# Optimization experiments

Hardware: AMD Instinct MI355X
Metric: run time of the kernel (lower is better)

The kernel has to match this reference:

```python
import jax, jax.numpy as jnp
import numpy as np

N, F_IN, H1, H2, HEADS, E = 8192, 512, 128, 64, 3, 262144
NEG_SLOPE = 0.2  # PyG GATConv default negative_slope


def _add_self_loops(src, dst, n):
    loop = jnp.arange(n, dtype=src.dtype)
    return jnp.concatenate([src, loop]), jnp.concatenate([dst, loop])


def _gcn_conv(x, src, dst, W, b, n):
    # PyG GCNConv: h = x @ W, add self-loops, symmetric D^-1/2 A D^-1/2 aggregation, + bias
    h = x @ W
    s, d = _add_self_loops(src, dst, n)
    deg = jax.ops.segment_sum(jnp.ones(s.shape, h.dtype), d, num_segments=n)
    dinv = jnp.where(deg > 0, jax.lax.rsqrt(deg), 0.0)
    norm = dinv[s] * dinv[d]  # [E']
    return jax.ops.segment_sum(h[s] * norm[:, None], d, num_segments=n) + b


def _gat_conv(x, src, dst, W, a_src, a_dst, b, n, heads, concat):
    # PyG GATConv: per-head linear, LeakyReLU attention logits, segment softmax over
    # incoming edges per destination node, weighted scatter-aggregate.
    out_dim = W.shape[1] // heads
    h = (x @ W).reshape(n, heads, out_dim)  # [N, H, D]
    s, d = _add_self_loops(src, dst, n)
    a_s = jnp.einsum('nhd,hd->nh', h, a_src)
    a_d = jnp.einsum('nhd,hd->nh', h, a_dst)
    e = jax.nn.leaky_relu(a_s[s] + a_d[d], NEG_SLOPE)  # [E', H]
    m = jax.ops.segment_max(e, d, num_segments=n)      # stable softmax per dst segment
    ex = jnp.exp(e - m[d])
    den = jax.ops.segment_sum(ex, d, num_segments=n)
    msg = h[s] * (ex / den[d])[..., None]              # [E', H, D]
    out = jax.ops.segment_sum(msg, d, num_segments=n)  # [N, H, D]
    if concat:
        return out.reshape(n, heads * out_dim) + b
    return out.mean(axis=1) + b


def _forward(x, edge_index, gcn_W1, gcn_b1, gcn_Wmu, gcn_bmu, gcn_Wlv, gcn_blv,
             gat_W1, gat_as1, gat_ad1, gat_b1,
             gat_Wmu, gat_asmu, gat_admu, gat_bmu,
             gat_Wlv, gat_aslv, gat_adlv, gat_blv,
             eps_gcn, eps_gat):
    src, dst = edge_index[0], edge_index[1]
    n = x.shape[0]
    mu_g = lv_g = z_g = None
    for i in range(gcn_W1.shape[0]):  # gcn branches
        h = jax.nn.relu(_gcn_conv(x, src, dst, gcn_W1[i], gcn_b1[i], n))
        mu = _gcn_conv(h, src, dst, gcn_Wmu[i], gcn_bmu[i], n)
        lv = _gcn_conv(h, src, dst, gcn_Wlv[i], gcn_blv[i], n)
        z = mu + eps_gcn[i] * jnp.exp(lv)  # faithful: logvar passed as logstd
        mu_g = mu if mu_g is None else jnp.maximum(mu_g, mu)
        lv_g = lv if lv_g is None else jnp.maximum(lv_g, lv)
        z_g = z if z_g is None else jnp.maximum(z_g, z)
    mu_a = lv_a = z_a = None
    for i in range(gat_W1.shape[0]):  # gat branches
        h = jax.nn.relu(_gat_conv(x, src, dst, gat_W1[i], gat_as1[i], gat_ad1[i], gat_b1[i], n, HEADS, True))
        mu = _gat_conv(h, src, dst, gat_Wmu[i], gat_asmu[i], gat_admu[i], gat_bmu[i], n, HEADS, False)
        lv = _gat_conv(h, src, dst, gat_Wlv[i], gat_aslv[i], gat_adlv[i], gat_blv[i], n, HEADS, False)
        z = mu + eps_gat[i] * jnp.exp(lv)
        mu_a = mu if mu_a is None else jnp.maximum(mu_a, mu)
        lv_a = lv if lv_a is None else jnp.maximum(lv_a, lv)
        z_a = z if z_a is None else jnp.maximum(z_a, z)
    mu_max = jnp.maximum(mu_g, mu_a)
    lv_max = jnp.maximum(lv_g, lv_a)
    z_max = jnp.maximum(z_g, z_a)
    adj = jax.nn.sigmoid(z_max @ z_max.T)  # InnerProductDecoder.forward_all(sigmoid=True)
    return adj, mu_max, lv_max


def setup_inputs():
    key = jax.random.key(0)
    ki = iter(jax.random.split(key, 32))
    p = lambda shape: jax.random.normal(next(ki), shape, dtype=jnp.float32) * 0.05
    x = jax.random.normal(next(ki), (N, F_IN), dtype=jnp.float32)
    edge_index = jax.random.randint(next(ki), (2, E), 0, N)
    return dict(
        x=x, edge_index=edge_index,
        gcn_W1=p((2, F_IN, H1)), gcn_b1=p((2, H1)),
        gcn_Wmu=p((2, H1, H2)), gcn_bmu=p((2, H2)),
        gcn_Wlv=p((2, H1, H2)), gcn_blv=p((2, H2)),
        gat_W1=p((2, F_IN, HEADS * H1)), gat_as1=p((2, HEADS, H1)),
        gat_ad1=p((2, HEADS, H1)), gat_b1=p((2, HEADS * H1)),
        gat_Wmu=p((2, HEADS * H1, HEADS * H2)), gat_asmu=p((2, HEADS, H2)),
        gat_admu=p((2, HEADS, H2)), gat_bmu=p((2, H2)),
        gat_Wlv=p((2, HEADS * H1, HEADS * H2)), gat_aslv=p((2, HEADS, H2)),
        gat_adlv=p((2, HEADS, H2)), gat_blv=p((2, H2)),
        eps_gcn=jax.random.normal(next(ki), (2, N, H2), dtype=jnp.float32),
        eps_gat=jax.random.normal(next(ki), (2, N, H2), dtype=jnp.float32),
    )


def reference(x, edge_index, gcn_W1, gcn_b1, gcn_Wmu, gcn_bmu, gcn_Wlv, gcn_blv,
              gat_W1, gat_as1, gat_ad1, gat_b1,
              gat_Wmu, gat_asmu, gat_admu, gat_bmu,
              gat_Wlv, gat_aslv, gat_adlv, gat_blv,
              eps_gcn, eps_gat):
    return _forward(x, edge_index, gcn_W1, gcn_b1, gcn_Wmu, gcn_bmu, gcn_Wlv, gcn_blv,
                    gat_W1, gat_as1, gat_ad1, gat_b1,
                    gat_Wmu, gat_asmu, gat_admu, gat_bmu,
                    gat_Wlv, gat_aslv, gat_adlv, gat_blv,
                    eps_gcn, eps_gat)
```

## Files before the change

### kernel.cpp

```cpp
#include <hip/hip_runtime.h>
#include <hip/hip_bf16.h>
#include <math.h>
#include <stddef.h>

#define NN 8192
#define NHEAD 3
#define NEG_SLOPE 0.2f

typedef __attribute__((ext_vector_type(8))) short short8;
typedef __attribute__((ext_vector_type(4))) float f32x4;

__device__ __forceinline__ float lrelu(float x) { return x > 0.f ? x : NEG_SLOPE * x; }
__device__ __forceinline__ float sigf(float x) { return 1.f / (1.f + __expf(-x)); }

__device__ __forceinline__ void splitbf(float x, unsigned short& hu, unsigned short& lu) {
    __hip_bfloat16 h = __float2bfloat16(x);
    float hf = __bfloat162float(h);
    __hip_bfloat16 l = __float2bfloat16(x - hf);
    hu = *reinterpret_cast<unsigned short*>(&h);
    lu = *reinterpret_cast<unsigned short*>(&l);
}
__device__ __forceinline__ unsigned short bfr(float x) {
    __hip_bfloat16 h = __float2bfloat16(x);
    return *reinterpret_cast<unsigned short*>(&h);
}
__device__ __forceinline__ unsigned int pack2(float a, float b) {
    return (unsigned int)bfr(a) | ((unsigned int)bfr(b) << 16);
}
__device__ __forceinline__ float2 unpk(unsigned int v) {
    unsigned int lo = v << 16;
    unsigned int hi = v & 0xffff0000u;
    float2 r;
    r.x = *reinterpret_cast<float*>(&lo);
    r.y = *reinterpret_cast<float*>(&hi);
    return r;
}
__device__ __forceinline__ float bf2f(unsigned short u) {
    unsigned int b = (unsigned int)u << 16;
    return *reinterpret_cast<float*>(&b);
}

__device__ __forceinline__ void gll16(const unsigned short* g, unsigned short* l) {
    __builtin_amdgcn_global_load_lds(
        (const __attribute__((address_space(1))) unsigned int*)g,
        (__attribute__((address_space(3))) unsigned int*)l, 16, 0, 0);
}

__global__ void k_zero(int* __restrict__ p, int n) {
    int i = blockIdx.x * blockDim.x + threadIdx.x;
    if (i < n) p[i] = 0;
}
__global__ void k_count(const int* __restrict__ dst, int* __restrict__ cnt, int E) {
    int i = blockIdx.x * blockDim.x + threadIdx.x;
    if (i < E) atomicAdd(&cnt[dst[i]], 1);
}
__global__ void k_dinv(const int* __restrict__ cnt, float* __restrict__ dinv) {
    int i = blockIdx.x * blockDim.x + threadIdx.x;
    if (i < NN) dinv[i] = rsqrtf((float)(cnt[i] + 1));
}
__global__ void k_scan(const int* __restrict__ cnt, int* __restrict__ row_ptr) {
    __shared__ int part[1024];
    int t = threadIdx.x;
    int base = t * 8;
    int loc[8];
    int s = 0;
    #pragma unroll
    for (int j = 0; j < 8; ++j) { loc[j] = s; s += cnt[base + j]; }
    part[t] = s;
    __syncthreads();
    for (int off = 1; off < 1024; off <<= 1) {
        int v = (t >= off) ? part[t - off] : 0;
        __syncthreads();
        part[t] += v;
        __syncthreads();
    }
    int pre = (t == 0) ? 0 : part[t - 1];
    #pragma unroll
    for (int j = 0; j < 8; ++j) row_ptr[base + j] = pre + loc[j];
    if (t == 1023) row_ptr[NN] = part[1023];
}
__global__ void k_fill(const int* __restrict__ src, const int* __restrict__ dst,
                       const int* __restrict__ row_ptr, int* __restrict__ cursor,
                       int* __restrict__ csr_src, int E) {
    int i = blockIdx.x * blockDim.x + threadIdx.x;
    if (i < E) {
        int d = dst[i];
        csr_src[row_ptr[d] + atomicAdd(&cursor[d], 1)] = src[i];
    }
}

__global__ void k_split_x(const float* __restrict__ x, unsigned short* __restrict__ x2) {
    int i = blockIdx.x * 256 + threadIdx.x;
    int m = i >> 7, k4 = (i & 127) * 4;
    float4 v = *(const float4*)(x + (size_t)m * 512 + k4);
    unsigned short h[4], l[4];
    splitbf(v.x, h[0], l[0]); splitbf(v.y, h[1], l[1]);
    splitbf(v.z, h[2], l[2]); splitbf(v.w, h[3], l[3]);
    ushort4 hv; hv.x = h[0]; hv.y = h[1]; hv.z = h[2]; hv.w = h[3];
    ushort4 lv; lv.x = l[0]; lv.y = l[1]; lv.z = l[2]; lv.w = l[3];
    *(ushort4*)&x2[(size_t)m * 1024 + k4] = hv;
    *(ushort4*)&x2[(size_t)m * 1024 + 512 + k4] = lv;
}

__global__ void k_wsplitT(const float* __restrict__ W, unsigned short* __restrict__ Wt,
                          int K, int N, size_t wt_z_stride, int noff, int noff_z) {
    int b = blockIdx.z;
    W += (size_t)b * K * N;
    Wt += (size_t)b * wt_z_stride;
    int rowbase = noff + b * noff_z;
    int k0 = blockIdx.x * 32, n0 = blockIdx.y * 32;
    __shared__ float tl[32][33];
    int tid = threadIdx.x;
    int r = tid >> 5, cc = tid & 31;
    #pragma unroll
    for (int c = 0; c < 4; ++c)
        tl[r + c * 8][cc] = W[(size_t)(k0 + r + c * 8) * N + n0 + cc];
    __syncthreads();
    #pragma unroll
    for (int c = 0; c < 4; ++c) {
        int n = r + c * 8, k = cc;
        float xv = tl[k][n];
        unsigned short h, l;
        splitbf(xv, h, l);
        size_t ro = (size_t)(rowbase + n0 + n) * 2 * K;
        Wt[ro + k0 + k] = h;
        Wt[ro + K + k0 + k] = l;
    }
}

template <int ROWS>
__device__ __forceinline__ void stage(const unsigned short* __restrict__ gbase, int lda,
                                      unsigned short* lds, int wid, int lane) {
    #pragma unroll
    for (int c = 0; c < ROWS / 32; ++c) {
        int chunk = c * 4 + wid;
        int row = chunk * 8 + (lane >> 3);
        int g = (lane & 7) ^ (row & 7);
        gll16(gbase + (size_t)row * lda + g * 8, lds + chunk * 512);
    }
}
__device__ __forceinline__ short8 fragr(const unsigned short* lds, int row, int kg) {
    return *(const short8*)(lds + row * 64 + ((kg ^ (row & 7)) * 8));
}

template <int EPI>
__global__ __launch_bounds__(256) void k_gemm2(
    const unsigned short* __restrict__ A2, size_t azs, int lda,
    const unsigned short* __restrict__ B2, size_t bzs, int ldb,
    void* __restrict__ Cv, size_t czs, int ldc, int K) {
    __shared__ __align__(16) unsigned short sAh[128 * 64];
    __shared__ __align__(16) unsigned short sAl[128 * 64];
    __shared__ __align__(16) unsigned short sBh[64 * 64];
    __shared__ __align__(16) unsigned short sBl[64 * 64];
    const int tid = threadIdx.x;
    const int wid = tid >> 6, lane = tid & 63;
    const int wr = wid >> 1, wc = wid & 1;
    const int lr = lane & 15, lg = lane >> 4;
    const int m0 = blockIdx.x * 128, n0 = blockIdx.y * 64;
    const int z = blockIdx.z;
    A2 += (size_t)z * azs;
    B2 += (size_t)z * bzs;

    const f32x4 zero4 = {0.f, 0.f, 0.f, 0.f};
    f32x4 acc[4][2];
    #pragma unroll
    for (int m = 0; m < 4; ++m)
        #pragma unroll
        for (int n = 0; n < 2; ++n) acc[m][n] = zero4;

    for (int k0 = 0; k0 < K; k0 += 64) {
        stage<128>(A2 + (size_t)m0 * lda + k0,     lda, sAh, wid, lane);
        stage<128>(A2 + (size_t)m0 * lda + K + k0, lda, sAl, wid, lane);
        stage<64> (B2 + (size_t)n0 * ldb + k0,     ldb, sBh, wid, lane);
        stage<64> (B2 + (size_t)n0 * ldb + K + k0, ldb, sBl, wid, lane);
        __syncthreads();
        #pragma unroll
        for (int ks = 0; ks < 2; ++ks) {
            const int kg = ks * 4 + lg;
            short8 ah[4], al[4], bh[2], bl[2];
            #pragma unroll
            for (int m = 0; m < 4; ++m) {
                int row = wr * 64 + m * 16 + lr;
                ah[m] = fragr(sAh, row, kg);
                al[m] = fragr(sAl, row, kg);
            }
            #pragma unroll
            for (int n = 0; n < 2; ++n) {
                int row = wc * 32 + n * 16 + lr;
                bh[n] = fragr(sBh, row, kg);
                bl[n] = fragr(sBl, row, kg);
            }
            #pragma unroll
            for (int m = 0; m < 4; ++m)
                #pragma unroll
                for (int n = 0; n < 2; ++n) {
                    acc[m][n] = __builtin_amdgcn_mfma_f32_16x16x32_bf16(ah[m], bh[n], acc[m][n], 0, 0, 0);
                    acc[m][n] = __builtin_amdgcn_mfma_f32_16x16x32_bf16(al[m], bh[n], acc[m][n], 0, 0, 0);
                    acc[m][n] = __builtin_amdgcn_mfma_f32_16x16x32_bf16(ah[m], bl[n], acc[m][n], 0, 0, 0);
                }
        }
        __syncthreads();
    }
    #pragma unroll
    for (int m = 0; m < 4; ++m)
        #pragma unroll
        for (int n = 0; n < 2; ++n)
            #pragma unroll
            for (int j = 0; j < 4; ++j) {
                int row = m0 + wr * 64 + m * 16 + lg * 4 + j;
                int col = n0 + wc * 32 + n * 16 + lr;
                float o = acc[m][n][j];
                if (EPI == 1) {
                    ((float*)Cv + (size_t)z * czs)[(size_t)row * ldc + col] = sigf(o);
                } else if (EPI == 2) {
                    ((unsigned short*)Cv + (size_t)z * czs)[(size_t)row * ldc + col] = bfr(o);
                } else {
                    ((float*)Cv + (size_t)z * czs)[(size_t)row * ldc + col] = o;
                }
            }
}

__global__ void k_gcn_a1(const unsigned int* __restrict__ xwb, const float* __restrict__ dinv,
                         const int* __restrict__ rp, const int* __restrict__ cs,
                         const float* __restrict__ b1, unsigned int* __restrict__ hb) {
    int d = blockIdx.x;
    int t = threadIdx.x;
    float dd = dinv[d];
    float2 sv = unpk(xwb[(size_t)d * 128 + t]);
    float a0 = dd * sv.x, a1 = dd * sv.y;
    int e0 = rp[d], e1 = rp[d + 1];
    int j = e0;
    for (; j + 4 <= e1; j += 4) {
        int s0 = cs[j], s1 = cs[j + 1], s2 = cs[j + 2], s3 = cs[j + 3];
        float w0 = dinv[s0], w1 = dinv[s1], w2 = dinv[s2], w3 = dinv[s3];
        float2 v0 = unpk(xwb[(size_t)s0 * 128 + t]);
        float2 v1 = unpk(xwb[(size_t)s1 * 128 + t]);
        float2 v2 = unpk(xwb[(size_t)s2 * 128 + t]);
        float2 v3 = unpk(xwb[(size_t)s3 * 128 + t]);
        a0 += w0 * v0.x + w1 * v1.x + w2 * v2.x + w3 * v3.x;
        a1 += w0 * v0.y + w1 * v1.y + w2 * v2.y + w3 * v3.y;
    }
    for (; j < e1; ++j) {
        int s = cs[j];
        float w = dinv[s];
        float2 v = unpk(xwb[(size_t)s * 128 + t]);
        a0 += w * v.x;
        a1 += w * v.y;
    }
    float o0 = fmaxf(dd * a0 + b1[2 * t], 0.f);
    float o1 = fmaxf(dd * a1 + b1[2 * t + 1], 0.f);
    hb[(size_t)d * 128 + t] = pack2(o0, o1);
}

__global__ void k_gcn_a2(const unsigned int* __restrict__ hb, const float* __restrict__ dinv,
                         const int* __restrict__ rp, const int* __restrict__ cs,
                         unsigned int* __restrict__ hA2u) {
    int d = blockIdx.x;
    int t = threadIdx.x;
    float dd = dinv[d];
    float2 sv = unpk(hb[(size_t)d * 128 + t]);
    float a0 = dd * sv.x, a1 = dd * sv.y;
    int e0 = rp[d], e1 = rp[d + 1];
    int j = e0;
    for (; j + 4 <= e1; j += 4) {
        int s0 = cs[j], s1 = cs[j + 1], s2 = cs[j + 2], s3 = cs[j + 3];
        float w0 = dinv[s0], w1 = dinv[s1], w2 = dinv[s2], w3 = dinv[s3];
        float2 v0 = unpk(hb[(size_t)s0 * 128 + t]);
        float2 v1 = unpk(hb[(size_t)s1 * 128 + t]);
        float2 v2 = unpk(hb[(size_t)s2 * 128 + t]);
        float2 v3 = unpk(hb[(size_t)s3 * 128 + t]);
        a0 += w0 * v0.x + w1 * v1.x + w2 * v2.x + w3 * v3.x;
        a1 += w0 * v0.y + w1 * v1.y + w2 * v2.y + w3 * v3.y;
    }
    for (; j < e1; ++j) {
        int s = cs[j];
        float w = dinv[s];
        float2 v = unpk(hb[(size_t)s * 128 + t]);
        a0 += w * v.x;
        a1 += w * v.y;
    }
    float o0 = dd * a0, o1 = dd * a1;
    int br = t >> 6, cu = t & 63;
    unsigned short h0, l0, h1, l1;
    splitbf(o0, h0, l0);
    splitbf(o1, h1, l1);
    hA2u[(size_t)d * 256 + br * 128 + cu] = (unsigned int)h0 | ((unsigned int)h1 << 16);
    hA2u[(size_t)d * 256 + br * 128 + 64 + cu] = (unsigned int)l0 | ((unsigned int)l1 << 16);
}

__global__ void k_gat_log1(const unsigned int* __restrict__ xwb, const float* __restrict__ a_s,
                           const float* __restrict__ a_d, float* __restrict__ as_n,
                           float* __restrict__ ad_n) {
    int br = blockIdx.z;
    int n = blockIdx.x;
    int hd = threadIdx.x >> 6, lane = threadIdx.x & 63;
    const unsigned int* hp = xwb + (size_t)n * 384 + br * 192 + hd * 64;
    const float* av = a_s + br * 384 + hd * 128;
    const float* dv = a_d + br * 384 + hd * 128;
    float2 f = unpk(hp[lane]);
    float ss = f.x * av[2 * lane] + f.y * av[2 * lane + 1];
    float sd = f.x * dv[2 * lane] + f.y * dv[2 * lane + 1];
    #pragma unroll
    for (int off = 32; off; off >>= 1) {
        ss += __shfl_down(ss, off);
        sd += __shfl_down(sd, off);
    }
    if (lane == 0) {
        as_n[(size_t)br * NN * 3 + n * 3 + hd] = ss;
        ad_n[(size_t)br * NN * 3 + n * 3 + hd] = sd;
    }
}

__global__ void k_gat_log2(const unsigned short* __restrict__ h2gb, const float* __restrict__ asmu,
                           const float* __restrict__ aslv, const float* __restrict__ admu,
                           const float* __restrict__ adlv, float* __restrict__ as_n,
                           float* __restrict__ ad_n) {
    int zz = blockIdx.z;
    int br = zz >> 1, mt = zz & 1;
    int n = blockIdx.x;
    int hd = threadIdx.x >> 6, lane = threadIdx.x & 63;
    const unsigned short* hp = h2gb + (size_t)br * NN * 384 + (size_t)n * 384 + mt * 192 + hd * 64;
    const float* av = (mt ? aslv : asmu) + br * 192 + hd * 64;
    const float* dv = (mt ? adlv : admu) + br * 192 + hd * 64;
    float hv = bf2f(hp[lane]);
    float ss = hv * av[lane];
    float sd = hv * dv[lane];
    #pragma unroll
    for (int off = 32; off; off >>= 1) {
        ss += __shfl_down(ss, off);
        sd += __shfl_down(sd, off);
    }
    if (lane == 0) {
        as_n[(size_t)zz * NN * 3 + n * 3 + hd] = ss;
        ad_n[(size_t)zz * NN * 3 + n * 3 + hd] = sd;
    }
}

__global__ void k_gat_attn(const float* __restrict__ as_n, const float* __restrict__ ad_n,
                           const int* __restrict__ rp, const int* __restrict__ cs,
                           float* __restrict__ w_csr, float* __restrict__ w_self, int E3) {
    int zz = blockIdx.z;
    as_n += (size_t)zz * NN * 3;
    ad_n += (size_t)zz * NN * 3;
    w_csr += (size_t)zz * E3;
    w_self += (size_t)zz * NN * 3;
    int d = blockIdx.x;
    int hd = threadIdx.x >> 6, lane = threadIdx.x & 63;
    int e0 = rp[d], e1 = rp[d + 1];
    float add = ad_n[d * 3 + hd];
    float eself = lrelu(as_n[d * 3 + hd] + add);
    float mx = eself;
    for (int j = e0 + lane; j < e1; j += 64) {
        float e = lrelu(as_n[cs[j] * 3 + hd] + add);
        w_csr[(size_t)j * 3 + hd] = e;
        mx = fmaxf(mx, e);
    }
    #pragma unroll
    for (int off = 32; off; off >>= 1) mx = fmaxf(mx, __shfl_xor(mx, off));
    float sm = (lane == 0) ? __expf(eself - mx) : 0.f;
    for (int j = e0 + lane; j < e1; j += 64)
        sm += __expf(w_csr[(size_t)j * 3 + hd] - mx);
    #pragma unroll
    for (int off = 32; off; off >>= 1) sm += __shfl_xor(sm, off);
    float inv = 1.f / sm;
    if (lane == 0) w_self[d * 3 + hd] = __expf(eself - mx) * inv;
    for (int j = e0 + lane; j < e1; j += 64)
        w_csr[(size_t)j * 3 + hd] = __expf(w_csr[(size_t)j * 3 + hd] - mx) * inv;
}

__global__ void k_gat_agg1(const unsigned int* __restrict__ xwb, const float* __restrict__ w_csr,
                           const float* __restrict__ w_self, const int* __restrict__ rp,
                           const int* __restrict__ cs, const float* __restrict__ b1,
                           unsigned int* __restrict__ h1su, int E3) {
    int d = blockIdx.x;
    int t = threadIdx.x;
    int br = t >= 192 ? 1 : 0;
    int cu = t - br * 192;
    int hd = cu >> 6;
    const float* wc = w_csr + (size_t)br * E3;
    float ws = w_self[(size_t)br * NN * 3 + d * 3 + hd];
    float2 sv = unpk(xwb[(size_t)d * 384 + t]);
    float a0 = ws * sv.x, a1 = ws * sv.y;
    int e0 = rp[d], e1 = rp[d + 1];
    int j = e0;
    for (; j + 4 <= e1; j += 4) {
        int s0 = cs[j], s1 = cs[j + 1], s2 = cs[j + 2], s3 = cs[j + 3];
        float w0 = wc[(size_t)(j + 0) * 3 + hd];
        float w1 = wc[(size_t)(j + 1) * 3 + hd];
        float w2 = wc[(size_t)(j + 2) * 3 + hd];
        float w3 = wc[(size_t)(j + 3) * 3 + hd];
        float2 v0 = unpk(xwb[(size_t)s0 * 384 + t]);
        float2 v1 = unpk(xwb[(size_t)s1 * 384 + t]);
        float2 v2 = unpk(xwb[(size_t)s2 * 384 + t]);
        float2 v3 = unpk(xwb[(size_t)s3 * 384 + t]);
        a0 += w0 * v0.x + w1 * v1.x + w2 * v2.x + w3 * v3.x;
        a1 += w0 * v0.y + w1 * v1.y + w2 * v2.y + w3 * v3.y;
    }
    for (; j < e1; ++j) {
        int s = cs[j];
        float w = wc[(size_t)j * 3 + hd];
        float2 v = unpk(xwb[(size_t)s * 384 + t]);
        a0 += w * v.x;
        a1 += w * v.y;
    }
    float o0 = fmaxf(a0 + b1[br * 384 + 2 * cu], 0.f);
    float o1 = fmaxf(a1 + b1[br * 384 + 2 * cu + 1], 0.f);
    unsigned short h0, l0, h1, l1;
    splitbf(o0, h0, l0);
    splitbf(o1, h1, l1);
    h1su[(size_t)d * 768 + br * 384 + cu] = (unsigned int)h0 | ((unsigned int)h1 << 16);
    h1su[(size_t)d * 768 + br * 384 + 192 + cu] = (unsigned int)l0 | ((unsigned int)l1 << 16);
}

__global__ void k_gat_agg2(const unsigned int* __restrict__ h2gu, const float* __restrict__ w_csr,
                           const float* __restrict__ w_self, const int* __restrict__ rp,
                           const int* __restrict__ cs, const float* __restrict__ bmu,
                           const float* __restrict__ blv, float* __restrict__ mt_gat, int E3) {
    int br = blockIdx.z;
    int d = blockIdx.x;
    int t = threadIdx.x;
    int mt = t >= 96 ? 1 : 0;
    int cu = t - mt * 96;
    int hd = cu >> 5;
    const unsigned int* hp = h2gu + (size_t)br * NN * 192;
    const float* wc = w_csr + (size_t)(br * 2 + mt) * E3;
    float ws = w_self[(size_t)(br * 2 + mt) * NN * 3 + d * 3 + hd];
    float2 sv = unpk(hp[(size_t)d * 192 + t]);
    float a0 = ws * sv.x, a1 = ws * sv.y;
    int e0 = rp[d], e1 = rp[d + 1];
    int j = e0;
    for (; j + 4 <= e1; j += 4) {
        int s0 = cs[j], s1 = cs[j + 1], s2 = cs[j + 2], s3 = cs[j + 3];
        float w0 = wc[(size_t)(j + 0) * 3 + hd];
        float w1 = wc[(size_t)(j + 1) * 3 + hd];
        float w2 = wc[(size_t)(j + 2) * 3 + hd];
        float w3 = wc[(size_t)(j + 3) * 3 + hd];
        float2 v0 = unpk(hp[(size_t)s0 * 192 + t]);
        float2 v1 = unpk(hp[(size_t)s1 * 192 + t]);
        float2 v2 = unpk(hp[(size_t)s2 * 192 + t]);
        float2 v3 = unpk(hp[(size_t)s3 * 192 + t]);
        a0 += w0 * v0.x + w1 * v1.x + w2 * v2.x + w3 * v3.x;
        a1 += w0 * v0.y + w1 * v1.y + w2 * v2.y + w3 * v3.y;
    }
    for (; j < e1; ++j) {
        int s = cs[j];
        float w = wc[(size_t)j * 3 + hd];
        float2 v = unpk(hp[(size_t)s * 192 + t]);
        a0 += w * v.x;
        a1 += w * v.y;
    }
    __shared__ float red[384];
    red[2 * t] = a0;
    red[2 * t + 1] = a1;
    __syncthreads();
    if (t < 128) {
        int mt2 = t >> 6, dd = t & 63;
        float tot = red[mt2 * 192 + dd] + red[mt2 * 192 + 64 + dd] + red[mt2 * 192 + 128 + dd];
        const float* bias = mt2 ? blv : bmu;
        float o = tot * (1.f / 3.f) + bias[br * 64 + dd];
        mt_gat[((size_t)(br * 2 + mt2) * NN + d) * 64 + dd] = o;
    }
}

__global__ void k_finalize(const float* __restrict__ muv_gcn, const float* __restrict__ gcn_bmu,
                           const float* __restrict__ gcn_blv, const float* __restrict__ mt_gat,
                           const float* __restrict__ eps_gcn, const float* __restrict__ eps_gat,
                           float* __restrict__ mu_o, float* __restrict__ lv_o,
                           unsigned short* __restrict__ z2) {
    int i = blockIdx.x * 256 + threadIdx.x;
    int d = i >> 6, c = i & 63;
    const size_t NN64 = (size_t)NN * 64;
    float mu, lv, zm;
    {
        float m = muv_gcn[(size_t)d * 128 + c] + gcn_bmu[c];
        float l = muv_gcn[(size_t)d * 128 + 64 + c] + gcn_blv[c];
        float z = m + eps_gcn[i] * __expf(l);
        mu = m; lv = l; zm = z;
    }
    {
        float m = muv_gcn[NN64 * 2 + (size_t)d * 128 + c] + gcn_bmu[64 + c];
        float l = muv_gcn[NN64 * 2 + (size_t)d * 128 + 64 + c] + gcn_blv[64 + c];
        float z = m + eps_gcn[NN64 + i] * __expf(l);
        mu = fmaxf(mu, m); lv = fmaxf(lv, l); zm = fmaxf(zm, z);
    }
    #pragma unroll
    for (int br = 0; br < 2; ++br) {
        float m = mt_gat[(size_t)(br * 2 + 0) * NN64 + i];
        float l = mt_gat[(size_t)(br * 2 + 1) * NN64 + i];
        float z = m + eps_gat[(size_t)br * NN64 + i] * __expf(l);
        mu = fmaxf(mu, m); lv = fmaxf(lv, l); zm = fmaxf(zm, z);
    }
    mu_o[i] = mu;
    lv_o[i] = lv;
    unsigned short hh, ll;
    splitbf(zm, hh, ll);
    z2[(size_t)d * 128 + c] = hh;
    z2[(size_t)d * 128 + 64 + c] = ll;
}

extern "C" void kernel_launch(void* const* d_in, const int* in_sizes, int n_in,
                              void* d_out, int out_size, void* d_ws, size_t ws_size,
                              hipStream_t stream) {
    const float* x  = (const float*)d_in[0];
    const int*   ei = (const int*)d_in[1];
    const int E = in_sizes[1] / 2;
    const int E3 = E * 3;
    const int* src = ei;
    const int* dst = ei + E;

    const float* gcn_W1  = (const float*)d_in[2];
    const float* gcn_b1  = (const float*)d_in[3];
    const float* gcn_Wmu = (const float*)d_in[4];
    const float* gcn_bmu = (const float*)d_in[5];
    const float* gcn_Wlv = (const float*)d_in[6];
    const float* gcn_blv = (const float*)d_in[7];
    const float* gat_W1  = (const float*)d_in[8];
    const float* gat_as1 = (const float*)d_in[9];
    const float* gat_ad1 = (const float*)d_in[10];
    const float* gat_b1  = (const float*)d_in[11];
    const float* gat_Wmu = (const float*)d_in[12];
    const float* gat_asmu= (const float*)d_in[13];
    const float* gat_admu= (const float*)d_in[14];
    const float* gat_bmu = (const float*)d_in[15];
    const float* gat_Wlv = (const float*)d_in[16];
    const float* gat_aslv= (const float*)d_in[17];
    const float* gat_adlv= (const float*)d_in[18];
    const float* gat_blv = (const float*)d_in[19];
    const float* eps_gcn = (const float*)d_in[20];
    const float* eps_gat = (const float*)d_in[21];

    char* p = (char*)d_ws;
    auto alloc = [&](size_t bytes) {
        void* r = (void*)p;
        p += (bytes + 255) & ~(size_t)255;
        return r;
    };
    int*   cnt     = (int*)alloc((size_t)NN * 4);
    int*   cursor  = (int*)alloc((size_t)NN * 4);
    int*   row_ptr = (int*)alloc((size_t)(NN + 1) * 4);
    int*   csr_src = (int*)alloc((size_t)E * 4);
    float* dinv    = (float*)alloc((size_t)NN * 4);
    float* as_n1   = (float*)alloc((size_t)2 * NN * 3 * 4);
    float* ad_n1   = (float*)alloc((size_t)2 * NN * 3 * 4);
    float* wself1  = (float*)alloc((size_t)2 * NN * 3 * 4);
    float* wcsr1   = (float*)alloc((size_t)2 * E3 * 4);
    float* as_n2   = (float*)alloc((size_t)4 * NN * 3 * 4);
    float* ad_n2   = (float*)alloc((size_t)4 * NN * 3 * 4);
    float* wself2  = (float*)alloc((size_t)4 * NN * 3 * 4);
    float* wcsr2   = (float*)alloc((size_t)4 * E3 * 4);
    unsigned short* x2       = (unsigned short*)alloc((size_t)NN * 1024 * 2);
    unsigned short* wt_gcn1  = (unsigned short*)alloc((size_t)256 * 1024 * 2);
    unsigned short* wt_gcnmuv= (unsigned short*)alloc((size_t)2 * 128 * 256 * 2);
    unsigned short* wt_gat1  = (unsigned short*)alloc((size_t)768 * 1024 * 2);
    unsigned short* wt_gatmuv= (unsigned short*)alloc((size_t)2 * 384 * 768 * 2);
    unsigned int* xwb  = (unsigned int*)alloc((size_t)NN * 384 * 4);
    unsigned int* hb   = (unsigned int*)alloc((size_t)NN * 128 * 4);
    unsigned int* hA2u = (unsigned int*)alloc((size_t)NN * 256 * 4);
    float* muv_gcn = (float*)alloc((size_t)2 * NN * 128 * 4);
    unsigned int* h1su = (unsigned int*)alloc((size_t)NN * 768 * 4);
    unsigned short* h2gb = (unsigned short*)alloc((size_t)2 * NN * 384 * 2);
    float* mt_gat  = (float*)alloc((size_t)4 * NN * 64 * 4);
    unsigned short* z2 = (unsigned short*)alloc((size_t)NN * 128 * 2);

    float* adj  = (float*)d_out;
    float* mu_o = adj + (size_t)NN * NN;
    float* lv_o = mu_o + (size_t)NN * 64;

    k_zero<<<(2 * NN + 255) / 256, 256, 0, stream>>>(cnt, 2 * NN);
    k_count<<<(E + 255) / 256, 256, 0, stream>>>(dst, cnt, E);
    k_dinv<<<(NN + 255) / 256, 256, 0, stream>>>(cnt, dinv);
    k_scan<<<1, 1024, 0, stream>>>(cnt, row_ptr);
    k_fill<<<(E + 255) / 256, 256, 0, stream>>>(src, dst, row_ptr, cursor, csr_src, E);

    k_split_x<<<NN * 512 / 4 / 256, 256, 0, stream>>>(x, x2);
    k_wsplitT<<<dim3(16, 4, 2), 256, 0, stream>>>(gcn_W1, wt_gcn1, 512, 128, 0, 0, 128);
    k_wsplitT<<<dim3(4, 2, 2), 256, 0, stream>>>(gcn_Wmu, wt_gcnmuv, 128, 64,
                                                 (size_t)128 * 256, 0, 0);
    k_wsplitT<<<dim3(4, 2, 2), 256, 0, stream>>>(gcn_Wlv, wt_gcnmuv, 128, 64,
                                                 (size_t)128 * 256, 64, 0);
    k_wsplitT<<<dim3(16, 12, 2), 256, 0, stream>>>(gat_W1, wt_gat1, 512, 384, 0, 0, 384);
    k_wsplitT<<<dim3(12, 6, 2), 256, 0, stream>>>(gat_Wmu, wt_gatmuv, 384, 192,
                                                  (size_t)384 * 768, 0, 0);
    k_wsplitT<<<dim3(12, 6, 2), 256, 0, stream>>>(gat_Wlv, wt_gatmuv, 384, 192,
                                                  (size_t)384 * 768, 192, 0);

    k_gemm2<2><<<dim3(64, 4, 1), 256, 0, stream>>>(x2, 0, 1024, wt_gcn1, 0, 1024,
                                                   xwb, 0, 256, 512);
    k_gcn_a1<<<NN, 128, 0, stream>>>(xwb, dinv, row_ptr, csr_src, gcn_b1, hb);
    k_gcn_a2<<<NN, 128, 0, stream>>>(hb, dinv, row_ptr, csr_src, hA2u);
    k_gemm2<0><<<dim3(64, 2, 2), 256, 0, stream>>>((const unsigned short*)hA2u, 256, 512,
                                                   wt_gcnmuv, (size_t)128 * 256, 256,
                                                   muv_gcn, (size_t)NN * 128, 128, 128);

    k_gemm2<2><<<dim3(64, 12, 1), 256, 0, stream>>>(x2, 0, 1024, wt_gat1, 0, 1024,
                                                    xwb, 0, 768, 512);
    k_gat_log1<<<dim3(NN, 1, 2), 192, 0, stream>>>(xwb, gat_as1, gat_ad1, as_n1, ad_n1);
    k_gat_attn<<<dim3(NN, 1, 2), 192, 0, stream>>>(as_n1, ad_n1, row_ptr, csr_src,
                                                   wcsr1, wself1, E3);
    k_gat_agg1<<<NN, 384, 0, stream>>>(xwb, wcsr1, wself1, row_ptr, csr_src, gat_b1,
                                       h1su, E3);
    k_gemm2<2><<<dim3(64, 6, 2), 256, 0, stream>>>((const unsigned short*)h1su, 768, 1536,
                                                   wt_gatmuv, (size_t)384 * 768, 768,
                                                   h2gb, (size_t)NN * 384, 384, 384);
    k_gat_log2<<<dim3(NN, 1, 4), 192, 0, stream>>>(h2gb, gat_asmu, gat_aslv, gat_admu,
                                                   gat_adlv, as_n2, ad_n2);
    k_gat_attn<<<dim3(NN, 1, 4), 192, 0, stream>>>(as_n2, ad_n2, row_ptr, csr_src,
                                                   wcsr2, wself2, E3);
    k_gat_agg2<<<dim3(NN, 1, 2), 192, 0, stream>>>((const unsigned int*)h2gb, wcsr2, wself2,
                                                   row_ptr, csr_src, gat_bmu, gat_blv,
                                                   mt_gat, E3);

    k_finalize<<<NN * 64 / 256, 256, 0, stream>>>(muv_gcn, gcn_bmu, gcn_blv, mt_gat,
                                                  eps_gcn, eps_gat, mu_o, lv_o, z2);
    k_gemm2<1><<<dim3(64, 128, 1), 256, 0, stream>>>(z2, 0, 128, z2, 0, 128,
                                                     adj, 0, NN, 64);
}
```

Measured before the change: 390.2 us.

## Switch intermediate GEMMs from split-bf16 three-term to single fp16 MFMA

Replaces the hi/lo bf16 split (three MFMAs per tile) with a single fp16 term for the feature GEMMs, keeping three-term split only for the final z·zᵀ adjacency GEMM. This halves the staged operand traffic and removes two thirds of MFMA work in those GEMMs and halves weight/activation buffers. The aggregation kernels are rewritten to process four fp16 values per thread with uint2 loads, and gat_agg2 merges both branches into one block. Accuracy drops because of fp16 range and mantissa limits compared with the split representation.

```diff
diff --git a/kernel.cpp b/kernel.cpp
--- a/kernel.cpp
+++ b/kernel.cpp
@@ -4,40 +4,40 @@
 #include <stddef.h>
 
 #define NN 8192
-#define NHEAD 3
 #define NEG_SLOPE 0.2f
 
-typedef __attribute__((ext_vector_type(8))) short short8;
+typedef _Float16 h8 __attribute__((ext_vector_type(8)));
 typedef __attribute__((ext_vector_type(4))) float f32x4;
 
 __device__ __forceinline__ float lrelu(float x) { return x > 0.f ? x : NEG_SLOPE * x; }
 __device__ __forceinline__ float sigf(float x) { return 1.f / (1.f + __expf(-x)); }
 
-__device__ __forceinline__ void splitbf(float x, unsigned short& hu, unsigned short& lu) {
-    __hip_bfloat16 h = __float2bfloat16(x);
-    float hf = __bfloat162float(h);
-    __hip_bfloat16 l = __float2bfloat16(x - hf);
-    hu = *reinterpret_cast<unsigned short*>(&h);
-    lu = *reinterpret_cast<unsigned short*>(&l);
-}
-__device__ __forceinline__ unsigned short bfr(float x) {
-    __hip_bfloat16 h = __float2bfloat16(x);
-    return *reinterpret_cast<unsigned short*>(&h);
-}
-__device__ __forceinline__ unsigned int pack2(float a, float b) {
-    return (unsigned int)bfr(a) | ((unsigned int)bfr(b) << 16);
-}
-__device__ __forceinline__ float2 unpk(unsigned int v) {
-    unsigned int lo = v << 16;
-    unsigned int hi = v & 0xffff0000u;
+__device__ __forceinline__ unsigned short f16b(float x) {
+    _Float16 h = (_Float16)x;
+    unsigned short u;
+    __builtin_memcpy(&u, &h, 2);
+    return u;
+}
+__device__ __forceinline__ float f16f(unsigned short u) {
+    _Float16 h;
+    __builtin_memcpy(&h, &u, 2);
+    return (float)h;
+}
+__device__ __forceinline__ void splith(float x, unsigned short& hu, unsigned short& lu) {
+    _Float16 h = (_Float16)x;
+    float hf = (float)h;
+    _Float16 l = (_Float16)(x - hf);
+    __builtin_memcpy(&hu, &h, 2);
+    __builtin_memcpy(&lu, &l, 2);
+}
+__device__ __forceinline__ float2 unpkh(unsigned int v) {
     float2 r;
-    r.x = *reinterpret_cast<float*>(&lo);
-    r.y = *reinterpret_cast<float*>(&hi);
+    r.x = f16f((unsigned short)(v & 0xffffu));
+    r.y = f16f((unsigned short)(v >> 16));
     return r;
 }
-__device__ __forceinline__ float bf2f(unsigned short u) {
-    unsigned int b = (unsigned int)u << 16;
-    return *reinterpret_cast<float*>(&b);
+__device__ __forceinline__ unsigned int packh(float a, float b) {
+    return (unsigned int)f16b(a) | ((unsigned int)f16b(b) << 16);
 }
 
 __device__ __forceinline__ void gll16(const unsigned short* g, unsigned short* l) {
@@ -89,21 +89,17 @@
     }
 }
 
-__global__ void k_split_x(const float* __restrict__ x, unsigned short* __restrict__ x2) {
+__global__ void k_cvt_x(const float* __restrict__ x, unsigned short* __restrict__ xh) {
     int i = blockIdx.x * 256 + threadIdx.x;
     int m = i >> 7, k4 = (i & 127) * 4;
     float4 v = *(const float4*)(x + (size_t)m * 512 + k4);
-    unsigned short h[4], l[4];
-    splitbf(v.x, h[0], l[0]); splitbf(v.y, h[1], l[1]);
-    splitbf(v.z, h[2], l[2]); splitbf(v.w, h[3], l[3]);
-    ushort4 hv; hv.x = h[0]; hv.y = h[1]; hv.z = h[2]; hv.w = h[3];
-    ushort4 lv; lv.x = l[0]; lv.y = l[1]; lv.z = l[2]; lv.w = l[3];
-    *(ushort4*)&x2[(size_t)m * 1024 + k4] = hv;
-    *(ushort4*)&x2[(size_t)m * 1024 + 512 + k4] = lv;
-}
-
-__global__ void k_wsplitT(const float* __restrict__ W, unsigned short* __restrict__ Wt,
-                          int K, int N, size_t wt_z_stride, int noff, int noff_z) {
+    ushort4 o;
+    o.x = f16b(v.x); o.y = f16b(v.y); o.z = f16b(v.z); o.w = f16b(v.w);
+    *(ushort4*)&xh[(size_t)m * 512 + k4] = o;
+}
+
+__global__ void k_wT(const float* __restrict__ W, unsigned short* __restrict__ Wt,
+                     int K, int N, size_t wt_z_stride, int noff, int noff_z) {
     int b = blockIdx.z;
     W += (size_t)b * K * N;
     Wt += (size_t)b * wt_z_stride;
@@ -119,12 +115,7 @@
     #pragma unroll
     for (int c = 0; c < 4; ++c) {
         int n = r + c * 8, k = cc;
-        float xv = tl[k][n];
-        unsigned short h, l;
-        splitbf(xv, h, l);
-        size_t ro = (size_t)(rowbase + n0 + n) * 2 * K;
-        Wt[ro + k0 + k] = h;
-        Wt[ro + K + k0 + k] = l;
+        Wt[(size_t)(rowbase + n0 + n) * K + k0 + k] = f16b(tl[k][n]);
     }
 }
 
@@ -139,19 +130,19 @@
         gll16(gbase + (size_t)row * lda + g * 8, lds + chunk * 512);
     }
 }
-__device__ __forceinline__ short8 fragr(const unsigned short* lds, int row, int kg) {
-    return *(const short8*)(lds + row * 64 + ((kg ^ (row & 7)) * 8));
-}
-
-template <int EPI>
+__device__ __forceinline__ h8 fragrh(const unsigned short* lds, int row, int kg) {
+    return *(const h8*)(lds + row * 64 + ((kg ^ (row & 7)) * 8));
+}
+
+template <int TERMS, int EPI>
 __global__ __launch_bounds__(256) void k_gemm2(
     const unsigned short* __restrict__ A2, size_t azs, int lda,
     const unsigned short* __restrict__ B2, size_t bzs, int ldb,
     void* __restrict__ Cv, size_t czs, int ldc, int K) {
     __shared__ __align__(16) unsigned short sAh[128 * 64];
-    __shared__ __align__(16) unsigned short sAl[128 * 64];
     __shared__ __align__(16) unsigned short sBh[64 * 64];
-    __shared__ __align__(16) unsigned short sBl[64 * 64];
+    __shared__ __align__(16) unsigned short sAl[(TERMS == 3) ? 128 * 64 : 8];
+    __shared__ __align__(16) unsigned short sBl[(TERMS == 3) ? 64 * 64 : 8];
     const int tid = threadIdx.x;
     const int wid = tid >> 6, lane = tid & 63;
     const int wr = wid >> 1, wc = wid & 1;
@@ -169,34 +160,38 @@
         for (int n = 0; n < 2; ++n) acc[m][n] = zero4;
 
     for (int k0 = 0; k0 < K; k0 += 64) {
-        stage<128>(A2 + (size_t)m0 * lda + k0,     lda, sAh, wid, lane);
-        stage<128>(A2 + (size_t)m0 * lda + K + k0, lda, sAl, wid, lane);
-        stage<64> (B2 + (size_t)n0 * ldb + k0,     ldb, sBh, wid, lane);
-        stage<64> (B2 + (size_t)n0 * ldb + K + k0, ldb, sBl, wid, lane);
+        stage<128>(A2 + (size_t)m0 * lda + k0, lda, sAh, wid, lane);
+        stage<64> (B2 + (size_t)n0 * ldb + k0, ldb, sBh, wid, lane);
+        if (TERMS == 3) {
+            stage<128>(A2 + (size_t)m0 * lda + K + k0, lda, sAl, wid, lane);
+            stage<64> (B2 + (size_t)n0 * ldb + K + k0, ldb, sBl, wid, lane);
+        }
         __syncthreads();
         #pragma unroll
         for (int ks = 0; ks < 2; ++ks) {
             const int kg = ks * 4 + lg;
-            short8 ah[4], al[4], bh[2], bl[2];
+            h8 ah[4], al[4], bh[2], bl[2];
             #pragma unroll
             for (int m = 0; m < 4; ++m) {
                 int row = wr * 64 + m * 16 + lr;
-                ah[m] = fragr(sAh, row, kg);
-                al[m] = fragr(sAl, row, kg);
+                ah[m] = fragrh(sAh, row, kg);
+                if (TERMS == 3) al[m] = fragrh(sAl, row, kg);
             }
             #pragma unroll
             for (int n = 0; n < 2; ++n) {
                 int row = wc * 32 + n * 16 + lr;
-                bh[n] = fragr(sBh, row, kg);
-                bl[n] = fragr(sBl, row, kg);
+                bh[n] = fragrh(sBh, row, kg);
+                if (TERMS == 3) bl[n] = fragrh(sBl, row, kg);
             }
             #pragma unroll
             for (int m = 0; m < 4; ++m)
                 #pragma unroll
                 for (int n = 0; n < 2; ++n) {
-                    acc[m][n] = __builtin_amdgcn_mfma_f32_16x16x32_bf16(ah[m], bh[n], acc[m][n], 0, 0, 0);
-                    acc[m][n] = __builtin_amdgcn_mfma_f32_16x16x32_bf16(al[m], bh[n], acc[m][n], 0, 0, 0);
-                    acc[m][n] = __builtin_amdgcn_mfma_f32_16x16x32_bf16(ah[m], bl[n], acc[m][n], 0, 0, 0);
+                    acc[m][n] = __builtin_amdgcn_mfma_f32_16x16x32_f16(ah[m], bh[n], acc[m][n], 0, 0, 0);
+                    if (TERMS == 3) {
+                        acc[m][n] = __builtin_amdgcn_mfma_f32_16x16x32_f16(al[m], bh[n], acc[m][n], 0, 0, 0);
+                        acc[m][n] = __builtin_amdgcn_mfma_f32_16x16x32_f16(ah[m], bl[n], acc[m][n], 0, 0, 0);
+                    }
                 }
         }
         __syncthreads();
@@ -213,91 +208,112 @@
                 if (EPI == 1) {
                     ((float*)Cv + (size_t)z * czs)[(size_t)row * ldc + col] = sigf(o);
                 } else if (EPI == 2) {
-                    ((unsigned short*)Cv + (size_t)z * czs)[(size_t)row * ldc + col] = bfr(o);
+                    ((unsigned short*)Cv + (size_t)z * czs)[(size_t)row * ldc + col] = f16b(o);
                 } else {
                     ((float*)Cv + (size_t)z * czs)[(size_t)row * ldc + col] = o;
                 }
             }
 }
 
-__global__ void k_gcn_a1(const unsigned int* __restrict__ xwb, const float* __restrict__ dinv,
+__global__ void k_gcn_a1(const uint2* __restrict__ xw2, const float* __restrict__ dinv,
                          const int* __restrict__ rp, const int* __restrict__ cs,
-                         const float* __restrict__ b1, unsigned int* __restrict__ hb) {
+                         const float* __restrict__ b1, uint2* __restrict__ hb2) {
     int d = blockIdx.x;
     int t = threadIdx.x;
     float dd = dinv[d];
-    float2 sv = unpk(xwb[(size_t)d * 128 + t]);
-    float a0 = dd * sv.x, a1 = dd * sv.y;
+    uint2 sv = xw2[(size_t)d * 64 + t];
+    float2 s0 = unpkh(sv.x), s1 = unpkh(sv.y);
+    float a0 = dd * s0.x, a1 = dd * s0.y, a2 = dd * s1.x, a3 = dd * s1.y;
     int e0 = rp[d], e1 = rp[d + 1];
     int j = e0;
     for (; j + 4 <= e1; j += 4) {
-        int s0 = cs[j], s1 = cs[j + 1], s2 = cs[j + 2], s3 = cs[j + 3];
-        float w0 = dinv[s0], w1 = dinv[s1], w2 = dinv[s2], w3 = dinv[s3];
-        float2 v0 = unpk(xwb[(size_t)s0 * 128 + t]);
-        float2 v1 = unpk(xwb[(size_t)s1 * 128 + t]);
-        float2 v2 = unpk(xwb[(size_t)s2 * 128 + t]);
-        float2 v3 = unpk(xwb[(size_t)s3 * 128 + t]);
-        a0 += w0 * v0.x + w1 * v1.x + w2 * v2.x + w3 * v3.x;
-        a1 += w0 * v0.y + w1 * v1.y + w2 * v2.y + w3 * v3.y;
+        int i0 = cs[j], i1 = cs[j + 1], i2 = cs[j + 2], i3 = cs[j + 3];
+        float w0 = dinv[i0], w1 = dinv[i1], w2 = dinv[i2], w3 = dinv[i3];
+        uint2 v0 = xw2[(size_t)i0 * 64 + t];
+        uint2 v1 = xw2[(size_t)i1 * 64 + t];
+        uint2 v2 = xw2[(size_t)i2 * 64 + t];
+        uint2 v3 = xw2[(size_t)i3 * 64 + t];
+        float2 p;
+        p = unpkh(v0.x); a0 += w0 * p.x; a1 += w0 * p.y;
+        p = unpkh(v0.y); a2 += w0 * p.x; a3 += w0 * p.y;
+        p = unpkh(v1.x); a0 += w1 * p.x; a1 += w1 * p.y;
+        p = unpkh(v1.y); a2 += w1 * p.x; a3 += w1 * p.y;
+        p = unpkh(v2.x); a0 += w2 * p.x; a1 += w2 * p.y;
+        p = unpkh(v2.y); a2 += w2 * p.x; a3 += w2 * p.y;
+        p = unpkh(v3.x); a0 += w3 * p.x; a1 += w3 * p.y;
+        p = unpkh(v3.y); a2 += w3 * p.x; a3 += w3 * p.y;
     }
     for (; j < e1; ++j) {
         int s = cs[j];
         float w = dinv[s];
-        float2 v = unpk(xwb[(size_t)s * 128 + t]);
-        a0 += w * v.x;
-        a1 += w * v.y;
-    }
-    float o0 = fmaxf(dd * a0 + b1[2 * t], 0.f);
-    float o1 = fmaxf(dd * a1 + b1[2 * t + 1], 0.f);
-    hb[(size_t)d * 128 + t] = pack2(o0, o1);
-}
-
-__global__ void k_gcn_a2(const unsigned int* __restrict__ hb, const float* __restrict__ dinv,
+        uint2 v = xw2[(size_t)s * 64 + t];
+        float2 p;
+        p = unpkh(v.x); a0 += w * p.x; a1 += w * p.y;
+        p = unpkh(v.y); a2 += w * p.x; a3 += w * p.y;
+    }
+    int c = 4 * t;
+    float o0 = fmaxf(dd * a0 + b1[c], 0.f);
+    float o1 = fmaxf(dd * a1 + b1[c + 1], 0.f);
+    float o2 = fmaxf(dd * a2 + b1[c + 2], 0.f);
+    float o3 = fmaxf(dd * a3 + b1[c + 3], 0.f);
+    uint2 o;
+    o.x = packh(o0, o1);
+    o.y = packh(o2, o3);
+    hb2[(size_t)d * 64 + t] = o;
+}
+
+__global__ void k_gcn_a2(const uint2* __restrict__ hb2, const float* __restrict__ dinv,
                          const int* __restrict__ rp, const int* __restrict__ cs,
-                         unsigned int* __restrict__ hA2u) {
+                         uint2* __restrict__ hA2) {
     int d = blockIdx.x;
     int t = threadIdx.x;
     float dd = dinv[d];
-    float2 sv = unpk(hb[(size_t)d * 128 + t]);
-    float a0 = dd * sv.x, a1 = dd * sv.y;
+    uint2 sv = hb2[(size_t)d * 64 + t];
+    float2 s0 = unpkh(sv.x), s1 = unpkh(sv.y);
+    float a0 = dd * s0.x, a1 = dd * s0.y, a2 = dd * s1.x, a3 = dd * s1.y;
     int e0 = rp[d], e1 = rp[d + 1];
     int j = e0;
     for (; j + 4 <= e1; j += 4) {
-        int s0 = cs[j], s1 = cs[j + 1], s2 = cs[j + 2], s3 = cs[j + 3];
-        float w0 = dinv[s0], w1 = dinv[s1], w2 = dinv[s2], w3 = dinv[s3];
-        float2 v0 = unpk(hb[(size_t)s0 * 128 + t]);
-        float2 v1 = unpk(hb[(size_t)s1 * 128 + t]);
-        float2 v2 = unpk(hb[(size_t)s2 * 128 + t]);
-        float2 v3 = unpk(hb[(size_t)s3 * 128 + t]);
-        a0 += w0 * v0.x + w1 * v1.x + w2 * v2.x + w3 * v3.x;
-        a1 += w0 * v0.y + w1 * v1.y + w2 * v2.y + w3 * v3.y;
+        int i0 = cs[j], i1 = cs[j + 1], i2 = cs[j + 2], i3 = cs[j + 3];
+        float w0 = dinv[i0], w1 = dinv[i1], w2 = dinv[i2], w3 = dinv[i3];
+        uint2 v0 = hb2[(size_t)i0 * 64 + t];
+        uint2 v1 = hb2[(size_t)i1 * 64 + t];
+        uint2 v2 = hb2[(size_t)i2 * 64 + t];
+        uint2 v3 = hb2[(size_t)i3 * 64 + t];
+        float2 p;
+        p = unpkh(v0.x); a0 += w0 * p.x; a1 += w0 * p.y;
+        p = unpkh(v0.y); a2 += w0 * p.x; a3 += w0 * p.y;
+        p = unpkh(v1.x); a0 += w1 * p.x; a1 += w1 * p.y;
+        p = unpkh(v1.y); a2 += w1 * p.x; a3 += w1 * p.y;
+        p = unpkh(v2.x); a0 += w2 * p.x; a1 += w2 * p.y;
+        p = unpkh(v2.y); a2 += w2 * p.x; a3 += w2 * p.y;
+        p = unpkh(v3.x); a0 += w3 * p.x; a1 += w3 * p.y;
+        p = unpkh(v3.y); a2 += w3 * p.x; a3 += w3 * p.y;
     }
     for (; j < e1; ++j) {
         int s = cs[j];
         float w = dinv[s];
-        float2 v = unpk(hb[(size_t)s * 128 + t]);
-        a0 += w * v.x;
-        a1 += w * v.y;
-    }
-    float o0 = dd * a0, o1 = dd * a1;
-    int br = t >> 6, cu = t & 63;
-    unsigned short h0, l0, h1, l1;
-    splitbf(o0, h0, l0);
-    splitbf(o1, h1, l1);
-    hA2u[(size_t)d * 256 + br * 128 + cu] = (unsigned int)h0 | ((unsigned int)h1 << 16);
-    hA2u[(size_t)d * 256 + br * 128 + 64 + cu] = (unsigned int)l0 | ((unsigned int)l1 << 16);
-}
-
-__global__ void k_gat_log1(const unsigned int* __restrict__ xwb, const float* __restrict__ a_s,
+        uint2 v = hb2[(size_t)s * 64 + t];
+        float2 p;
+        p = unpkh(v.x); a0 += w * p.x; a1 += w * p.y;
+        p = unpkh(v.y); a2 += w * p.x; a3 += w * p.y;
+    }
+    uint2 o;
+    o.x = packh(dd * a0, dd * a1);
+    o.y = packh(dd * a2, dd * a3);
+    hA2[(size_t)d * 64 + t] = o;
+}
+
+__global__ void k_gat_log1(const unsigned int* __restrict__ xwu, const float* __restrict__ a_s,
                            const float* __restrict__ a_d, float* __restrict__ as_n,
                            float* __restrict__ ad_n) {
     int br = blockIdx.z;
     int n = blockIdx.x;
     int hd = threadIdx.x >> 6, lane = threadIdx.x & 63;
-    const unsigned int* hp = xwb + (size_t)n * 384 + br * 192 + hd * 64;
+    const unsigned int* hp = xwu + (size_t)n * 384 + br * 192 + hd * 64;
     const float* av = a_s + br * 384 + hd * 128;
     const float* dv = a_d + br * 384 + hd * 128;
-    float2 f = unpk(hp[lane]);
+    float2 f = unpkh(hp[lane]);
     float ss = f.x * av[2 * lane] + f.y * av[2 * lane + 1];
     float sd = f.x * dv[2 * lane] + f.y * dv[2 * lane + 1];
     #pragma unroll
@@ -322,7 +338,7 @@
     const unsigned short* hp = h2gb + (size_t)br * NN * 384 + (size_t)n * 384 + mt * 192 + hd * 64;
     const float* av = (mt ? aslv : asmu) + br * 192 + hd * 64;
     const float* dv = (mt ? adlv : admu) + br * 192 + hd * 64;
-    float hv = bf2f(hp[lane]);
+    float hv = f16f(hp[lane]);
     float ss = hv * av[lane];
     float sd = hv * dv[lane];
     #pragma unroll
@@ -368,97 +384,123 @@
         w_csr[(size_t)j * 3 + hd] = __expf(w_csr[(size_t)j * 3 + hd] - mx) * inv;
 }
 
-__global__ void k_gat_agg1(const unsigned int* __restrict__ xwb, const float* __restrict__ w_csr,
+__global__ void k_gat_agg1(const uint2* __restrict__ xw2, const float* __restrict__ w_csr,
                            const float* __restrict__ w_self, const int* __restrict__ rp,
                            const int* __restrict__ cs, const float* __restrict__ b1,
-                           unsigned int* __restrict__ h1su, int E3) {
+                           uint2* __restrict__ h1s2, int E3) {
     int d = blockIdx.x;
     int t = threadIdx.x;
-    int br = t >= 192 ? 1 : 0;
-    int cu = t - br * 192;
-    int hd = cu >> 6;
+    int br = t >= 96 ? 1 : 0;
+    int c = 4 * t - br * 384;
+    int hd = c >> 7;
     const float* wc = w_csr + (size_t)br * E3;
     float ws = w_self[(size_t)br * NN * 3 + d * 3 + hd];
-    float2 sv = unpk(xwb[(size_t)d * 384 + t]);
-    float a0 = ws * sv.x, a1 = ws * sv.y;
+    uint2 sv = xw2[(size_t)d * 192 + t];
+    float2 s0 = unpkh(sv.x), s1 = unpkh(sv.y);
+    float a0 = ws * s0.x, a1 = ws * s0.y, a2 = ws * s1.x, a3 = ws * s1.y;
     int e0 = rp[d], e1 = rp[d + 1];
     int j = e0;
     for (; j + 4 <= e1; j += 4) {
-        int s0 = cs[j], s1 = cs[j + 1], s2 = cs[j + 2], s3 = cs[j + 3];
+        int i0 = cs[j], i1 = cs[j + 1], i2 = cs[j + 2], i3 = cs[j + 3];
         float w0 = wc[(size_t)(j + 0) * 3 + hd];
         float w1 = wc[(size_t)(j + 1) * 3 + hd];
         float w2 = wc[(size_t)(j + 2) * 3 + hd];
         float w3 = wc[(size_t)(j + 3) * 3 + hd];
-        float2 v0 = unpk(xwb[(size_t)s0 * 384 + t]);
-        float2 v1 = unpk(xwb[(size_t)s1 * 384 + t]);
-        float2 v2 = unpk(xwb[(size_t)s2 * 384 + t]);
-        float2 v3 = unpk(xwb[(size_t)s3 * 384 + t]);
-        a0 += w0 * v0.x + w1 * v1.x + w2 * v2.x + w3 * v3.x;
-        a1 += w0 * v0.y + w1 * v1.y + w2 * v2.y + w3 * v3.y;
+        uint2 v0 = xw2[(size_t)i0 * 192 + t];
+        uint2 v1 = xw2[(size_t)i1 * 192 + t];
+        uint2 v2 = xw2[(size_t)i2 * 192 + t];
+        uint2 v3 = xw2[(size_t)i3 * 192 + t];
+        float2 p;
+        p = unpkh(v0.x); a0 += w0 * p.x; a1 += w0 * p.y;
+        p = unpkh(v0.y); a2 += w0 * p.x; a3 += w0 * p.y;
+        p = unpkh(v1.x); a0 += w1 * p.x; a1 += w1 * p.y;
+        p = unpkh(v1.y); a2 += w1 * p.x; a3 += w1 * p.y;
+        p = unpkh(v2.x); a0 += w2 * p.x; a1 += w2 * p.y;
+        p = unpkh(v2.y); a2 += w2 * p.x; a3 += w2 * p.y;
+        p = unpkh(v3.x); a0 += w3 * p.x; a1 += w3 * p.y;
+        p = unpkh(v3.y); a2 += w3 * p.x; a3 += w3 * p.y;
     }
     for (; j < e1; ++j) {
         int s = cs[j];
         float w = wc[(size_t)j * 3 + hd];
-        float2 v = unpk(xwb[(size_t)s * 384 + t]);
-        a0 += w * v.x;
-        a1 += w * v.y;
-    }
-    float o0 = fmaxf(a0 + b1[br * 384 + 2 * cu], 0.f);
-    float o1 = fmaxf(a1 + b1[br * 384 + 2 * cu + 1], 0.f);
-    unsigned short h0, l0, h1, l1;
-    splitbf(o0, h0, l0);
-    splitbf(o1, h1, l1);
-    h1su[(size_t)d * 768 + br * 384 + cu] = (unsigned int)h0 | ((unsigned int)h1 << 16);
-    h1su[(size_t)d * 768 + br * 384 + 192 + cu] = (unsigned int)l0 | ((unsigned int)l1 << 16);
-}
-
-__global__ void k_gat_agg2(const unsigned int* __restrict__ h2gu, const float* __restrict__ w_csr,
+        uint2 v = xw2[(size_t)s * 192 + t];
+        float2 p;
+        p = unpkh(v.x); a0 += w * p.x; a1 += w * p.y;
+        p = unpkh(v.y); a2 += w * p.x; a3 += w * p.y;
+    }
+    int cg = 4 * t;
+    float o0 = fmaxf(a0 + b1[cg], 0.f);
+    float o1 = fmaxf(a1 + b1[cg + 1], 0.f);
+    float o2 = fmaxf(a2 + b1[cg + 2], 0.f);
+    float o3 = fmaxf(a3 + b1[cg + 3], 0.f);
+    uint2 o;
+    o.x = packh(o0, o1);
+    o.y = packh(o2, o3);
+    h1s2[(size_t)d * 192 + t] = o;
+}
+
+__global__ void k_gat_agg2(const uint2* __restrict__ h2g2, const float* __restrict__ w_csr,
                            const float* __restrict__ w_self, const int* __restrict__ rp,
                            const int* __restrict__ cs, const float* __restrict__ bmu,
                            const float* __restrict__ blv, float* __restrict__ mt_gat, int E3) {
-    int br = blockIdx.z;
     int d = blockIdx.x;
     int t = threadIdx.x;
-    int mt = t >= 96 ? 1 : 0;
-    int cu = t - mt * 96;
-    int hd = cu >> 5;
-    const unsigned int* hp = h2gu + (size_t)br * NN * 192;
+    int br = t >= 96 ? 1 : 0;
+    int tb = t - br * 96;
+    int mt = tb >= 48 ? 1 : 0;
+    int c = 4 * tb - mt * 192;
+    int hd = c >> 6;
     const float* wc = w_csr + (size_t)(br * 2 + mt) * E3;
     float ws = w_self[(size_t)(br * 2 + mt) * NN * 3 + d * 3 + hd];
-    float2 sv = unpk(hp[(size_t)d * 192 + t]);
-    float a0 = ws * sv.x, a1 = ws * sv.y;
+    const uint2* hp = h2g2 + (size_t)br * NN * 96;
+    uint2 sv = hp[(size_t)d * 96 + tb];
+    float2 s0 = unpkh(sv.x), s1 = unpkh(sv.y);
+    float a0 = ws * s0.x, a1 = ws * s0.y, a2 = ws * s1.x, a3 = ws * s1.y;
     int e0 = rp[d], e1 = rp[d + 1];
     int j = e0;
     for (; j + 4 <= e1; j += 4) {
-        int s0 = cs[j], s1 = cs[j + 1], s2 = cs[j + 2], s3 = cs[j + 3];
+        int i0 = cs[j], i1 = cs[j + 1], i2 = cs[j + 2], i3 = cs[j + 3];
         float w0 = wc[(size_t)(j + 0) * 3 + hd];
         float w1 = wc[(size_t)(j + 1) * 3 + hd];
         float w2 = wc[(size_t)(j + 2) * 3 + hd];
         float w3 = wc[(size_t)(j + 3) * 3 + hd];
-        float2 v0 = unpk(hp[(size_t)s0 * 192 + t]);
-        float2 v1 = unpk(hp[(size_t)s1 * 192 + t]);
-        float2 v2 = unpk(hp[(size_t)s2 * 192 + t]);
-        float2 v3 = unpk(hp[(size_t)s3 * 192 + t]);
-        a0 += w0 * v0.x + w1 * v1.x + w2 * v2.x + w3 * v3.x;
-        a1 += w0 * v0.y + w1 * v1.y + w2 * v2.y + w3 * v3.y;
+        uint2 v0 = hp[(size_t)i0 * 96 + tb];
+        uint2 v1 = hp[(size_t)i1 * 96 + tb];
+        uint2 v2 = hp[(size_t)i2 * 96 + tb];
+        uint2 v3 = hp[(size_t)i3 * 96 + tb];
+        float2 p;
+        p = unpkh(v0.x); a0 += w0 * p.x; a1 += w0 * p.y;
+        p = unpkh(v0.y); a2 += w0 * p.x; a3 += w0 * p.y;
+        p = unpkh(v1.x); a0 += w1 * p.x; a1 += w1 * p.y;
+        p = unpkh(v1.y); a2 += w1 * p.x; a3 += w1 * p.y;
+        p = unpkh(v2.x); a0 += w2 * p.x; a1 += w2 * p.y;
+        p = unpkh(v2.y); a2 += w2 * p.x; a3 += w2 * p.y;
+        p = unpkh(v3.x); a0 += w3 * p.x; a1 += w3 * p.y;
+        p = unpkh(v3.y); a2 += w3 * p.x; a3 += w3 * p.y;
     }
     for (; j < e1; ++j) {
         int s = cs[j];
         float w = wc[(size_t)j * 3 + hd];
-        float2 v = unpk(hp[(size_t)s * 192 + t]);
-        a0 += w * v.x;
-        a1 += w * v.y;
-    }
-    __shared__ float red[384];
-    red[2 * t] = a0;
-    red[2 * t + 1] = a1;
+        uint2 v = hp[(size_t)s * 96 + tb];
+        float2 p;
+        p = unpkh(v.x); a0 += w * p.x; a1 += w * p.y;
+        p = unpkh(v.y); a2 += w * p.x; a3 += w * p.y;
+    }
+    __shared__ float red[768];
+    int rb = br * 384 + mt * 192 + c;
+    red[rb] = a0; red[rb + 1] = a1; red[rb + 2] = a2; red[rb + 3] = a3;
     __syncthreads();
     if (t < 128) {
-        int mt2 = t >> 6, dd = t & 63;
-        float tot = red[mt2 * 192 + dd] + red[mt2 * 192 + 64 + dd] + red[mt2 * 192 + 128 + dd];
-        const float* bias = mt2 ? blv : bmu;
-        float o = tot * (1.f / 3.f) + bias[br * 64 + dd];
-        mt_gat[((size_t)(br * 2 + mt2) * NN + d) * 64 + dd] = o;
+        #pragma unroll
+        for (int q = 0; q < 2; ++q) {
+            int o = t + q * 128;
+            int obr = o >> 7, omt = (o >> 6) & 1, dd = o & 63;
+            int base = obr * 384 + omt * 192;
+            float tot = red[base + dd] + red[base + 64 + dd] + red[base + 128 + dd];
+            const float* bias = omt ? blv : bmu;
+            float v = tot * (1.f / 3.f) + bias[obr * 64 + dd];
+            mt_gat[((size_t)(obr * 2 + omt) * NN + d) * 64 + dd] = v;
+        }
     }
 }
 
@@ -493,7 +535,7 @@
     mu_o[i] = mu;
     lv_o[i] = lv;
     unsigned short hh, ll;
-    splitbf(zm, hh, ll);
+    splith(zm, hh, ll);
     z2[(size_t)d * 128 + c] = hh;
     z2[(size_t)d * 128 + 64 + c] = ll;
 }
@@ -548,16 +590,16 @@
     float* ad_n2   = (float*)alloc((size_t)4 * NN * 3 * 4);
     float* wself2  = (float*)alloc((size_t)4 * NN * 3 * 4);
     float* wcsr2   = (float*)alloc((size_t)4 * E3 * 4);
-    unsigned short* x2       = (unsigned short*)alloc((size_t)NN * 1024 * 2);
-    unsigned short* wt_gcn1  = (unsigned short*)alloc((size_t)256 * 1024 * 2);
-    unsigned short* wt_gcnmuv= (unsigned short*)alloc((size_t)2 * 128 * 256 * 2);
-    unsigned short* wt_gat1  = (unsigned short*)alloc((size_t)768 * 1024 * 2);
-    unsigned short* wt_gatmuv= (unsigned short*)alloc((size_t)2 * 384 * 768 * 2);
-    unsigned int* xwb  = (unsigned int*)alloc((size_t)NN * 384 * 4);
-    unsigned int* hb   = (unsigned int*)alloc((size_t)NN * 128 * 4);
-    unsigned int* hA2u = (unsigned int*)alloc((size_t)NN * 256 * 4);
+    unsigned short* x2h      = (unsigned short*)alloc((size_t)NN * 512 * 2);
+    unsigned short* wt_gcn1  = (unsigned short*)alloc((size_t)256 * 512 * 2);
+    unsigned short* wt_gcnmuv= (unsigned short*)alloc((size_t)2 * 128 * 128 * 2);
+    unsigned short* wt_gat1  = (unsigned short*)alloc((size_t)768 * 512 * 2);
+    unsigned short* wt_gatmuv= (unsigned short*)alloc((size_t)2 * 384 * 384 * 2);
+    unsigned short* xwb  = (unsigned short*)alloc((size_t)NN * 768 * 2);
+    unsigned short* hb   = (unsigned short*)alloc((size_t)NN * 256 * 2);
+    unsigned short* hA   = (unsigned short*)alloc((size_t)NN * 256 * 2);
     float* muv_gcn = (float*)alloc((size_t)2 * NN * 128 * 4);
-    unsigned int* h1su = (unsigned int*)alloc((size_t)NN * 768 * 4);
+    unsigned short* h1s  = (unsigned short*)alloc((size_t)NN * 768 * 2);
     unsigned short* h2gb = (unsigned short*)alloc((size_t)2 * NN * 384 * 2);
     float* mt_gat  = (float*)alloc((size_t)4 * NN * 64 * 4);
     unsigned short* z2 = (unsigned short*)alloc((size_t)NN * 128 * 2);
@@ -572,46 +614,43 @@
     k_scan<<<1, 1024, 0, stream>>>(cnt, row_ptr);
     k_fill<<<(E + 255) / 256, 256, 0, stream>>>(src, dst, row_ptr, cursor, csr_src, E);
 
-    k_split_x<<<NN * 512 / 4 / 256, 256, 0, stream>>>(x, x2);
-    k_wsplitT<<<dim3(16, 4, 2), 256, 0, stream>>>(gcn_W1, wt_gcn1, 512, 128, 0, 0, 128);
-    k_wsplitT<<<dim3(4, 2, 2), 256, 0, stream>>>(gcn_Wmu, wt_gcnmuv, 128, 64,
-                                                 (size_t)128 * 256, 0, 0);
-    k_wsplitT<<<dim3(4, 2, 2), 256, 0, stream>>>(gcn_Wlv, wt_gcnmuv, 128, 64,
-                                                 (size_t)128 * 256, 64, 0);
-    k_wsplitT<<<dim3(16, 12, 2), 256, 0, stream>>>(gat_W1, wt_gat1, 512, 384, 0, 0, 384);
-    k_wsplitT<<<dim3(12, 6, 2), 256, 0, stream>>>(gat_Wmu, wt_gatmuv, 384, 192,
-                                                  (size_t)384 * 768, 0, 0);
-    k_wsplitT<<<dim3(12, 6, 2), 256, 0, stream>>>(gat_Wlv, wt_gatmuv, 384, 192,
-                                                  (size_t)384 * 768, 192, 0);
-
-    k_gemm2<2><<<dim3(64, 4, 1), 256, 0, stream>>>(x2, 0, 1024, wt_gcn1, 0, 1024,
-                                                   xwb, 0, 256, 512);
-    k_gcn_a1<<<NN, 128, 0, stream>>>(xwb, dinv, row_ptr, csr_src, gcn_b1, hb);
-    k_gcn_a2<<<NN, 128, 0, stream>>>(hb, dinv, row_ptr, csr_src, hA2u);
-    k_gemm2<0><<<dim3(64, 2, 2), 256, 0, stream>>>((const unsigned short*)hA2u, 256, 512,
-                                                   wt_gcnmuv, (size_t)128 * 256, 256,
-                                                   muv_gcn, (size_t)NN * 128, 128, 128);
-
-    k_gemm2<2><<<dim3(64, 12, 1), 256, 0, stream>>>(x2, 0, 1024, wt_gat1, 0, 1024,
-                                                    xwb, 0, 768, 512);
-    k_gat_log1<<<dim3(NN, 1, 2), 192, 0, stream>>>(xwb, gat_as1, gat_ad1, as_n1, ad_n1);
+    k_cvt_x<<<NN * 512 / 4 / 256, 256, 0, stream>>>(x, x2h);
+    k_wT<<<dim3(16, 4, 2), 256, 0, stream>>>(gcn_W1, wt_gcn1, 512, 128, 0, 0, 128);
+    k_wT<<<dim3(4, 2, 2), 256, 0, stream>>>(gcn_Wmu, wt_gcnmuv, 128, 64, (size_t)128 * 128, 0, 0);
+    k_wT<<<dim3(4, 2, 2), 256, 0, stream>>>(gcn_Wlv, wt_gcnmuv, 128, 64, (size_t)128 * 128, 64, 0);
+    k_wT<<<dim3(16, 12, 2), 256, 0, stream>>>(gat_W1, wt_gat1, 512, 384, 0, 0, 384);
+    k_wT<<<dim3(12, 6, 2), 256, 0, stream>>>(gat_Wmu, wt_gatmuv, 384, 192, (size_t)384 * 384, 0, 0);
+    k_wT<<<dim3(12, 6, 2), 256, 0, stream>>>(gat_Wlv, wt_gatmuv, 384, 192, (size_t)384 * 384, 192, 0);
+
+    k_gemm2<1, 2><<<dim3(64, 4, 1), 256, 0, stream>>>(x2h, 0, 512, wt_gcn1, 0, 512,
+                                                      xwb, 0, 256, 512);
+    k_gcn_a1<<<NN, 64, 0, stream>>>((const uint2*)xwb, dinv, row_ptr, csr_src, gcn_b1,
+                                    (uint2*)hb);
+    k_gcn_a2<<<NN, 64, 0, stream>>>((const uint2*)hb, dinv, row_ptr, csr_src, (uint2*)hA);
+    k_gemm2<1, 0><<<dim3(64, 2, 2), 256, 0, stream>>>(hA, 128, 256, wt_gcnmuv,
+                                                      (size_t)128 * 128, 128,
+                                                      muv_gcn, (size_t)NN * 128, 128, 128);
+
+    k_gemm2<1, 2><<<dim3(64, 12, 1), 256, 0, stream>>>(x2h, 0, 512, wt_gat1, 0, 512,
+                                                       xwb, 0, 768, 512);
+    k_gat_log1<<<dim3(NN, 1, 2), 192, 0, stream>>>((const unsigned int*)xwb, gat_as1,
+                                                   gat_ad1, as_n1, ad_n1);
     k_gat_attn<<<dim3(NN, 1, 2), 192, 0, stream>>>(as_n1, ad_n1, row_ptr, csr_src,
                                                    wcsr1, wself1, E3);
-    k_gat_agg1<<<NN, 384, 0, stream>>>(xwb, wcsr1, wself1, row_ptr, csr_src, gat_b1,
-                                       h1su, E3);
-    k_gemm2<2><<<dim3(64, 6, 2), 256, 0, stream>>>((const unsigned short*)h1su, 768, 1536,
-                                                   wt_gatmuv, (size_t)384 * 768, 768,
-                                                   h2gb, (size_t)NN * 384, 384, 384);
+    k_gat_agg1<<<NN, 192, 0, stream>>>((const uint2*)xwb, wcsr1, wself1, row_ptr, csr_src,
+                                       gat_b1, (uint2*)h1s, E3);
+    k_gemm2<1, 2><<<dim3(64, 6, 2), 256, 0, stream>>>(h1s, 384, 768, wt_gatmuv,
+                                                      (size_t)384 * 384, 384,
+                                                      h2gb, (size_t)NN * 384, 384, 384);
     k_gat_log2<<<dim3(NN, 1, 4), 192, 0, stream>>>(h2gb, gat_asmu, gat_aslv, gat_admu,
                                                    gat_adlv, as_n2, ad_n2);
     k_gat_attn<<<dim3(NN, 1, 4), 192, 0, stream>>>(as_n2, ad_n2, row_ptr, csr_src,
                                                    wcsr2, wself2, E3);
-    k_gat_agg2<<<dim3(NN, 1, 2), 192, 0, stream>>>((const unsigned int*)h2gb, wcsr2, wself2,
-                                                   row_ptr, csr_src, gat_bmu, gat_blv,
-                                                   mt_gat, E3);
+    k_gat_agg2<<<NN, 192, 0, stream>>>((const uint2*)h2gb, wcsr2, wself2, row_ptr, csr_src,
+                                       gat_bmu, gat_blv, mt_gat, E3);
 
     k_finalize<<<NN * 64 / 256, 256, 0, stream>>>(muv_gcn, gcn_bmu, gcn_blv, mt_gat,
                                                   eps_gcn, eps_gat, mu_o, lv_o, z2);
-    k_gemm2<1><<<dim3(64, 128, 1), 256, 0, stream>>>(z2, 0, 128, z2, 0, 128,
-                                                     adj, 0, NN, 64);
-}
+    k_gemm2<3, 1><<<dim3(64, 128, 1), 256, 0, stream>>>(z2, 0, 128, z2, 0, 128,
+                                                        adj, 0, NN, 64);
+}
```

After: 364.8 us. 1.07x faster.
